# Performance work log

Measured on AMD Instinct MI355X. Metric: run time of the kernel, lower is better.

The kernel has to match this reference:

```python
import jax, jax.numpy as jnp
import numpy as np

NODE_FEATURES = 256
HIDDEN = 32
N_NODES = 100000
N_EDGES = 3200000


def _glorot(key, shape):
    fan_in, fan_out = shape[-2], shape[-1]
    lim = (6.0 / (fan_in + fan_out)) ** 0.5
    return jax.random.uniform(key, shape, jnp.float32, -lim, lim)


def setup_inputs() -> dict:
    key = jax.random.key(0)
    ks = jax.random.split(key, 12)
    in_cat = NODE_FEATURES + HIDDEN  # DConv input is cat([X, H])
    x = jax.random.normal(ks[0], (N_NODES, NODE_FEATURES), jnp.float32)
    edge_index = jax.random.randint(ks[1], (2, N_EDGES), 0, N_NODES, jnp.int64)
    return {
        "x": x,
        "edge_index": edge_index,
        # DConv weights have shape (2, K=1, in, out); squeeze K -> (2, in, out)
        "w_z": _glorot(ks[2], (2, in_cat, HIDDEN)),
        "b_z": jnp.zeros((HIDDEN,), jnp.float32),
        "w_r": _glorot(ks[3], (2, in_cat, HIDDEN)),
        "b_r": jnp.zeros((HIDDEN,), jnp.float32),
        "w_h": _glorot(ks[4], (2, in_cat, HIDDEN)),
        "b_h": jnp.zeros((HIDDEN,), jnp.float32),
        # fc head, stored as [in, out]
        "fc1_w": _glorot(ks[5], (HIDDEN, HIDDEN)),
        "fc1_b": jnp.zeros((HIDDEN,), jnp.float32),
        "fc2_w": _glorot(ks[6], (HIDDEN, 1)),
        "fc2_b": jnp.zeros((1,), jnp.float32),
    }


def _dconv_k1(inp, w, b):
    # K=1 DConv: only the k=0 Chebyshev term for both diffusion directions,
    # i.e. no propagation over edges. H = X @ W_out + X @ W_in + bias.
    return inp @ (w[0] + w[1]) + b


def reference(x, edge_index, w_z, b_z, w_r, b_r, w_h, b_h, fc1_w, fc1_b, fc2_w, fc2_b):
    n = x.shape[0]
    h0 = jnp.zeros((n, HIDDEN), x.dtype)  # DCRNN called with H=None -> zeros
    xh0 = jnp.concatenate([x, h0], axis=1)  # [N, F+H]
    z = jax.nn.sigmoid(_dconv_k1(xh0, w_z, b_z))  # update gate
    r = jax.nn.sigmoid(_dconv_k1(xh0, w_r, b_r))  # reset gate
    xrh = jnp.concatenate([x, r * h0], axis=1)
    h_tilde = jnp.tanh(_dconv_k1(xrh, w_h, b_h))
    h = z * h0 + (1.0 - z) * h_tilde  # [N, 32]
    # fc head: Linear-ReLU-Dropout(eval=identity)-Linear-Sigmoid
    hidden = jax.nn.relu(h @ fc1_w + fc1_b)
    out = jax.nn.sigmoid(hidden @ fc2_w + fc2_b)  # [N, 1]
    return out
```

## Files before the change

kernel.cpp:

```cpp
#include <hip/hip_runtime.h>
#include <hip/hip_bf16.h>


#define NF    256
#define TILE  32
#define WPB   4
#define MB    (TILE * WPB)
#define NTHR  256
#define HSTR  36

typedef __attribute__((ext_vector_type(8)))  short  short8;
typedef __attribute__((ext_vector_type(16))) float  floatx16;

__device__ __forceinline__ unsigned f2bf(float f) {
    __hip_bfloat16 h = __float2bfloat16(f);
    return (unsigned)*(unsigned short*)&h;
}
__device__ __forceinline__ float fast_sigmoid(float v) {
    return 1.0f / (1.0f + __expf(-v));
}
__device__ __forceinline__ float fast_tanh(float v) {
    return 1.0f - 2.0f / (1.0f + __expf(2.0f * v));
}

__global__ void prep_W(const float* __restrict__ wz,
                       const float* __restrict__ wh,
                       unsigned short* __restrict__ Wf)
{
    int idx = blockIdx.x * blockDim.x + threadIdx.x;
    if (idx >= NF * 64) return;
    int j    = idx & 7;
    int lane = (idx >> 3) & 63;
    int nt   = (idx >> 9) & 1;
    int kt   = idx >> 10;
    int k = kt * 16 + (lane >> 5) * 8 + j;
    int o = nt * 32 + (lane & 31);
    const int PLANE = 288 * 32;
    float v;
    if (o < 32) v = wz[k * 32 + o]        + wz[PLANE + k * 32 + o];
    else        v = wh[k * 32 + (o - 32)] + wh[PLANE + k * 32 + (o - 32)];
    Wf[idx] = (unsigned short)f2bf(v);
}

__global__ void __launch_bounds__(NTHR, 3)
rgcn_main(const float* __restrict__ x,
          const unsigned short* __restrict__ Wf,
          const float* __restrict__ bz,
          const float* __restrict__ bh,
          const float* __restrict__ fc1w,
          const float* __restrict__ fc1b,
          const float* __restrict__ fc2w,
          const float* __restrict__ fc2b,
          float* __restrict__ out,
          int n_nodes)
{
    __shared__ float Hs[WPB * TILE * HSTR];

    const int tid   = threadIdx.x;
    const int lane  = tid & 63;
    const int wave  = tid >> 6;
    const int node0 = blockIdx.x * MB + wave * TILE;

    const int m    = lane & 31;
    const int koff = (lane >> 5) * 8;
    int gn_a = node0 + m;
    if (gn_a >= n_nodes) gn_a = n_nodes - 1;
    const float* xr = x + (size_t)gn_a * NF + koff;

    floatx16 acc0 = {};
    floatx16 acc1 = {};

#pragma unroll
    for (int kt = 0; kt < 16; ++kt) {
        float4 v0 = *(const float4*)(xr + kt * 16);
        float4 v1 = *(const float4*)(xr + kt * 16 + 4);
        const uint4* bp = (const uint4*)Wf + (size_t)(kt * 2) * 64 + lane;
        uint4 b0u = bp[0];
        uint4 b1u = bp[64];
        union { short8 s; unsigned u[4]; } a, b0, b1;
        a.u[0] = f2bf(v0.x) | (f2bf(v0.y) << 16);
        a.u[1] = f2bf(v0.z) | (f2bf(v0.w) << 16);
        a.u[2] = f2bf(v1.x) | (f2bf(v1.y) << 16);
        a.u[3] = f2bf(v1.z) | (f2bf(v1.w) << 16);
        b0.u[0] = b0u.x; b0.u[1] = b0u.y; b0.u[2] = b0u.z; b0.u[3] = b0u.w;
        b1.u[0] = b1u.x; b1.u[1] = b1u.y; b1.u[2] = b1u.z; b1.u[3] = b1u.w;
        acc0 = __builtin_amdgcn_mfma_f32_32x32x16_bf16(a.s, b0.s, acc0, 0, 0, 0);
        acc1 = __builtin_amdgcn_mfma_f32_32x32x16_bf16(a.s, b1.s, acc1, 0, 0, 0);
    }

    const int nc = lane & 31;
    const float bzn = bz[nc];
    const float bhn = bh[nc];
    float* Hw = Hs + wave * TILE * HSTR;
#pragma unroll
    for (int r = 0; r < 16; ++r) {
        int row = (r & 3) + 8 * (r >> 2) + 4 * (lane >> 5);
        float z = fast_sigmoid(acc0[r] + bzn);
        float t = fast_tanh   (acc1[r] + bhn);
        Hw[row * HSTR + nc] = (1.0f - z) * t;
    }
    __syncthreads();

    const int nl   = lane & 31;
    const int half = lane >> 5;
    const float* hp = Hw + nl * HSTR;
    float h[32];
#pragma unroll
    for (int q = 0; q < 8; ++q) {
        float4 v = *(const float4*)(hp + q * 4);
        h[q * 4 + 0] = v.x; h[q * 4 + 1] = v.y;
        h[q * 4 + 2] = v.z; h[q * 4 + 3] = v.w;
    }
    float part = 0.0f;
    for (int jj = 0; jj < 16; ++jj) {
        int j = (half << 4) + jj;
        float s = fc1b[j];
#pragma unroll
        for (int o = 0; o < 32; ++o)
            s = fmaf(h[o], fc1w[o * 32 + j], s);
        part = fmaf(fmaxf(s, 0.0f), fc2w[j], part);
    }
    part += __shfl_xor(part, 32);
    if (half == 0) {
        int gn = node0 + nl;
        if (gn < n_nodes)
            out[gn] = fast_sigmoid(part + fc2b[0]);
    }
}

extern "C" void kernel_launch(void* const* d_in, const int* in_sizes, int n_in,
                              void* d_out, int out_size, void* d_ws, size_t ws_size,
                              hipStream_t stream) {
    const float* x    = (const float*)d_in[0];
    const float* wz   = (const float*)d_in[2];
    const float* bz   = (const float*)d_in[3];
    const float* wh   = (const float*)d_in[6];
    const float* bh   = (const float*)d_in[7];
    const float* fc1w = (const float*)d_in[8];
    const float* fc1b = (const float*)d_in[9];
    const float* fc2w = (const float*)d_in[10];
    const float* fc2b = (const float*)d_in[11];
    float* out = (float*)d_out;
    unsigned short* Wf = (unsigned short*)d_ws;

    const int n = in_sizes[0] / NF;

    prep_W<<<(NF * 64 + 255) / 256, 256, 0, stream>>>(wz, wh, Wf);
    rgcn_main<<<(n + MB - 1) / MB, NTHR, 0, stream>>>(
        x, Wf, bz, bh, fc1w, fc1b, fc2w, fc2b, out, n);
}
```

Baseline: 209.5 us.

## Stage x tiles into LDS via direct global-to-LDS loads in K chunks

Replaces the per-lane strided float4 loads of x rows with global_load_lds instructions that copy 256-byte row chunks directly into shared memory, then reads MFMA A-operands from LDS. K is split into 4 chunks, each followed by block barriers, with a padded group stride to limit bank conflicts. Launch bounds occupancy hint is raised from 3 to 4. The aim is better coalesced HBM access for this bandwidth-bound GEMV-like kernel, at the cost of extra barriers and no overlap between loading and compute within a block.

```diff
diff --git a/kernel.cpp b/kernel.cpp
--- a/kernel.cpp
+++ b/kernel.cpp
@@ -2,15 +2,18 @@
 #include <hip/hip_bf16.h>
 
 
-#define NF    256
-#define TILE  32
-#define WPB   4
-#define MB    (TILE * WPB)
-#define NTHR  256
-#define HSTR  36
+#define NF     256
+#define TILE   32
+#define WPB    4
+#define MB     (TILE * WPB)
+#define NTHR   256
+#define GRP    1040
+#define HSTR   36
 
 typedef __attribute__((ext_vector_type(8)))  short  short8;
 typedef __attribute__((ext_vector_type(16))) float  floatx16;
+typedef __attribute__((address_space(1))) const unsigned int gu32;
+typedef __attribute__((address_space(3))) unsigned int       lu32;
 
 __device__ __forceinline__ unsigned f2bf(float f) {
     __hip_bfloat16 h = __float2bfloat16(f);
@@ -42,7 +45,7 @@
     Wf[idx] = (unsigned short)f2bf(v);
 }
 
-__global__ void __launch_bounds__(NTHR, 3)
+__global__ void __launch_bounds__(NTHR, 4)
 rgcn_main(const float* __restrict__ x,
           const unsigned short* __restrict__ Wf,
           const float* __restrict__ bz,
@@ -54,44 +57,66 @@
           float* __restrict__ out,
           int n_nodes)
 {
-    __shared__ float Hs[WPB * TILE * HSTR];
+    __shared__ __align__(16) char S[32 * GRP];
 
     const int tid   = threadIdx.x;
     const int lane  = tid & 63;
     const int wave  = tid >> 6;
-    const int node0 = blockIdx.x * MB + wave * TILE;
+    const int node0 = blockIdx.x * MB;
+    const int wb    = wave * TILE;
 
-    const int m    = lane & 31;
+    const int rsel = lane >> 4;
+    const int cb   = (lane & 15) * 16;
+
+    const int m    = wb + (lane & 31);
     const int koff = (lane >> 5) * 8;
-    int gn_a = node0 + m;
-    if (gn_a >= n_nodes) gn_a = n_nodes - 1;
-    const float* xr = x + (size_t)gn_a * NF + koff;
+    const char* arow = S + (m >> 2) * GRP + (m & 3) * 256;
 
     floatx16 acc0 = {};
     floatx16 acc1 = {};
 
 #pragma unroll
-    for (int kt = 0; kt < 16; ++kt) {
-        float4 v0 = *(const float4*)(xr + kt * 16);
-        float4 v1 = *(const float4*)(xr + kt * 16 + 4);
-        const uint4* bp = (const uint4*)Wf + (size_t)(kt * 2) * 64 + lane;
-        uint4 b0u = bp[0];
-        uint4 b1u = bp[64];
-        union { short8 s; unsigned u[4]; } a, b0, b1;
-        a.u[0] = f2bf(v0.x) | (f2bf(v0.y) << 16);
-        a.u[1] = f2bf(v0.z) | (f2bf(v0.w) << 16);
-        a.u[2] = f2bf(v1.x) | (f2bf(v1.y) << 16);
-        a.u[3] = f2bf(v1.z) | (f2bf(v1.w) << 16);
-        b0.u[0] = b0u.x; b0.u[1] = b0u.y; b0.u[2] = b0u.z; b0.u[3] = b0u.w;
-        b1.u[0] = b1u.x; b1.u[1] = b1u.y; b1.u[2] = b1u.z; b1.u[3] = b1u.w;
-        acc0 = __builtin_amdgcn_mfma_f32_32x32x16_bf16(a.s, b0.s, acc0, 0, 0, 0);
-        acc1 = __builtin_amdgcn_mfma_f32_32x32x16_bf16(a.s, b1.s, acc1, 0, 0, 0);
+    for (int c = 0; c < 4; ++c) {
+        if (c) __syncthreads();
+#pragma unroll
+        for (int i = 0; i < 8; ++i) {
+            int inst = wave * 8 + i;
+            int row  = node0 + inst * 4 + rsel;
+            if (row >= n_nodes) row = n_nodes - 1;
+            const char* g = (const char*)x + (size_t)row * (NF * 4)
+                          + c * 256 + cb;
+            char* lp = S + inst * GRP;
+            __builtin_amdgcn_global_load_lds((gu32*)g, (lu32*)lp, 16, 0, 0);
+        }
+        __syncthreads();
+
+#pragma unroll
+        for (int kt = 0; kt < 4; ++kt) {
+            int ktg = c * 4 + kt;
+            const float4* ap = (const float4*)(arow + (kt * 16 + koff) * 4);
+            float4 v0 = ap[0];
+            float4 v1 = ap[1];
+            const uint4* bp = (const uint4*)Wf + (size_t)(ktg * 2) * 64 + lane;
+            uint4 b0u = bp[0];
+            uint4 b1u = bp[64];
+            union { short8 s; unsigned u[4]; } a, b0, b1;
+            a.u[0] = f2bf(v0.x) | (f2bf(v0.y) << 16);
+            a.u[1] = f2bf(v0.z) | (f2bf(v0.w) << 16);
+            a.u[2] = f2bf(v1.x) | (f2bf(v1.y) << 16);
+            a.u[3] = f2bf(v1.z) | (f2bf(v1.w) << 16);
+            b0.u[0] = b0u.x; b0.u[1] = b0u.y; b0.u[2] = b0u.z; b0.u[3] = b0u.w;
+            b1.u[0] = b1u.x; b1.u[1] = b1u.y; b1.u[2] = b1u.z; b1.u[3] = b1u.w;
+            acc0 = __builtin_amdgcn_mfma_f32_32x32x16_bf16(a.s, b0.s, acc0, 0, 0, 0);
+            acc1 = __builtin_amdgcn_mfma_f32_32x32x16_bf16(a.s, b1.s, acc1, 0, 0, 0);
+        }
     }
 
+    __syncthreads();
+    float* Hs = (float*)S;
+    float* Hw = Hs + wave * TILE * HSTR;
     const int nc = lane & 31;
     const float bzn = bz[nc];
     const float bhn = bh[nc];
-    float* Hw = Hs + wave * TILE * HSTR;
 #pragma unroll
     for (int r = 0; r < 16; ++r) {
         int row = (r & 3) + 8 * (r >> 2) + 4 * (lane >> 5);
@@ -122,7 +147,7 @@
     }
     part += __shfl_xor(part, 32);
     if (half == 0) {
-        int gn = node0 + nl;
+        int gn = node0 + wb + nl;
         if (gn < n_nodes)
             out[gn] = fast_sigmoid(part + fc2b[0]);
     }
```

After: 205.3 us. 1.02x faster.

## Stage weights in LDS and double-buffer x loads in register chunks

Applied to the files above, without the earlier changes.

Each block first copies the packed bf16 weight fragments (32 KB) into shared memory, using a padded group stride to spread banks, so the MFMA loop reads B operands from LDS instead of global memory. The x row loads are split into four 64-element chunks and double-buffered in registers, with sched_barriers that force the next chunk's loads to issue before the current chunk's MFMAs. The block-wide __syncthreads after the H tile write becomes a per-wave lgkmcnt wait, since each wave only reads its own tile. In exchange the kernel uses about 33 KB more LDS per block and more registers, which can reduce occupancy under launch_bounds(256,3), and every block pays a preamble copy plus a barrier.

```diff
diff --git a/kernel.cpp b/kernel.cpp
--- a/kernel.cpp
+++ b/kernel.cpp
@@ -7,6 +7,7 @@
 #define WPB   4
 #define MB    (TILE * WPB)
 #define NTHR  256
+#define BGRP  1040
 #define HSTR  36
 
 typedef __attribute__((ext_vector_type(8)))  short  short8;
@@ -54,44 +55,75 @@
           float* __restrict__ out,
           int n_nodes)
 {
+    __shared__ __align__(16) char SB[32 * BGRP];
     __shared__ float Hs[WPB * TILE * HSTR];
 
     const int tid   = threadIdx.x;
     const int lane  = tid & 63;
     const int wave  = tid >> 6;
-    const int node0 = blockIdx.x * MB + wave * TILE;
+    const int node0 = blockIdx.x * MB;
 
-    const int m    = lane & 31;
-    const int koff = (lane >> 5) * 8;
-    int gn_a = node0 + m;
+    {
+        const uint4* src = (const uint4*)Wf;
+#pragma unroll
+        for (int i = 0; i < 8; ++i) {
+            int q = i * NTHR + tid;
+            uint4 v = src[q];
+            *(uint4*)(SB + (q >> 6) * BGRP + (q & 63) * 16) = v;
+        }
+    }
+    __syncthreads();
+
+    const int m  = lane & 31;
+    int gn_a = node0 + wave * TILE + m;
     if (gn_a >= n_nodes) gn_a = n_nodes - 1;
-    const float* xr = x + (size_t)gn_a * NF + koff;
+    const float* xr = x + (size_t)gn_a * NF + (lane >> 5) * 8;
 
     floatx16 acc0 = {};
     floatx16 acc1 = {};
 
+    float4 bufA[8], bufB[8];
+    const char* bl = SB + lane * 16;
+
 #pragma unroll
-    for (int kt = 0; kt < 16; ++kt) {
-        float4 v0 = *(const float4*)(xr + kt * 16);
-        float4 v1 = *(const float4*)(xr + kt * 16 + 4);
-        const uint4* bp = (const uint4*)Wf + (size_t)(kt * 2) * 64 + lane;
-        uint4 b0u = bp[0];
-        uint4 b1u = bp[64];
-        union { short8 s; unsigned u[4]; } a, b0, b1;
-        a.u[0] = f2bf(v0.x) | (f2bf(v0.y) << 16);
-        a.u[1] = f2bf(v0.z) | (f2bf(v0.w) << 16);
-        a.u[2] = f2bf(v1.x) | (f2bf(v1.y) << 16);
-        a.u[3] = f2bf(v1.z) | (f2bf(v1.w) << 16);
-        b0.u[0] = b0u.x; b0.u[1] = b0u.y; b0.u[2] = b0u.z; b0.u[3] = b0u.w;
-        b1.u[0] = b1u.x; b1.u[1] = b1u.y; b1.u[2] = b1u.z; b1.u[3] = b1u.w;
-        acc0 = __builtin_amdgcn_mfma_f32_32x32x16_bf16(a.s, b0.s, acc0, 0, 0, 0);
-        acc1 = __builtin_amdgcn_mfma_f32_32x32x16_bf16(a.s, b1.s, acc1, 0, 0, 0);
+    for (int t = 0; t < 8; ++t)
+        bufA[t] = *(const float4*)(xr + (t >> 1) * 16 + (t & 1) * 4);
+    __builtin_amdgcn_sched_barrier(0);
+
+#pragma unroll
+    for (int c = 0; c < 4; ++c) {
+        if (c < 3) {
+            float4* nb = ((c & 1) == 0) ? bufB : bufA;
+            const float* xc = xr + (c + 1) * 64;
+#pragma unroll
+            for (int t = 0; t < 8; ++t)
+                nb[t] = *(const float4*)(xc + (t >> 1) * 16 + (t & 1) * 4);
+            __builtin_amdgcn_sched_barrier(0);
+        }
+        const float4* cb = ((c & 1) == 0) ? bufA : bufB;
+#pragma unroll
+        for (int kt = 0; kt < 4; ++kt) {
+            float4 v0 = cb[kt * 2];
+            float4 v1 = cb[kt * 2 + 1];
+            int g = (c * 4 + kt) * 2;
+            uint4 b0u = *(const uint4*)(bl + (size_t)g * BGRP);
+            uint4 b1u = *(const uint4*)(bl + (size_t)(g + 1) * BGRP);
+            union { short8 s; unsigned u[4]; } a, b0, b1;
+            a.u[0] = f2bf(v0.x) | (f2bf(v0.y) << 16);
+            a.u[1] = f2bf(v0.z) | (f2bf(v0.w) << 16);
+            a.u[2] = f2bf(v1.x) | (f2bf(v1.y) << 16);
+            a.u[3] = f2bf(v1.z) | (f2bf(v1.w) << 16);
+            b0.u[0] = b0u.x; b0.u[1] = b0u.y; b0.u[2] = b0u.z; b0.u[3] = b0u.w;
+            b1.u[0] = b1u.x; b1.u[1] = b1u.y; b1.u[2] = b1u.z; b1.u[3] = b1u.w;
+            acc0 = __builtin_amdgcn_mfma_f32_32x32x16_bf16(a.s, b0.s, acc0, 0, 0, 0);
+            acc1 = __builtin_amdgcn_mfma_f32_32x32x16_bf16(a.s, b1.s, acc1, 0, 0, 0);
+        }
     }
 
+    float* Hw = Hs + wave * TILE * HSTR;
     const int nc = lane & 31;
     const float bzn = bz[nc];
     const float bhn = bh[nc];
-    float* Hw = Hs + wave * TILE * HSTR;
 #pragma unroll
     for (int r = 0; r < 16; ++r) {
         int row = (r & 3) + 8 * (r >> 2) + 4 * (lane >> 5);
@@ -99,7 +131,7 @@
         float t = fast_tanh   (acc1[r] + bhn);
         Hw[row * HSTR + nc] = (1.0f - z) * t;
     }
-    __syncthreads();
+    asm volatile("s_waitcnt lgkmcnt(0)" ::: "memory");
 
     const int nl   = lane & 31;
     const int half = lane >> 5;
@@ -122,7 +154,7 @@
     }
     part += __shfl_xor(part, 32);
     if (half == 0) {
-        int gn = node0 + nl;
+        int gn = node0 + wave * TILE + nl;
         if (gn < n_nodes)
             out[gn] = fast_sigmoid(part + fc2b[0]);
     }
```

New measurement: 203.4 us. -2.9%, faster.

## Split K across waves with LDS reduction and nontemporal x loads

Applied to the files above, without the earlier changes.

Each block now handles 64 nodes, and the four waves are split into two node tiles times two K-halves. Each wave runs half the MFMA K loop, and the partial accumulators are reduced through shared memory before the gate epilogue and FC head. The intent is more waves in flight per node and higher memory-level parallelism on the bandwidth-bound x read, helped by nontemporal loads and a raised occupancy hint. The cost is extra LDS traffic, two more barriers, and half the waves sitting idle during the epilogue.

```diff
diff --git a/kernel.cpp b/kernel.cpp
--- a/kernel.cpp
+++ b/kernel.cpp
@@ -4,13 +4,14 @@
 
 #define NF    256
 #define TILE  32
-#define WPB   4
-#define MB    (TILE * WPB)
+#define NPB   64
 #define NTHR  256
-#define HSTR  36
+#define CSTR  68
+#define HKT   8
 
 typedef __attribute__((ext_vector_type(8)))  short  short8;
 typedef __attribute__((ext_vector_type(16))) float  floatx16;
+typedef __attribute__((ext_vector_type(4)))  float  f32x4;
 
 __device__ __forceinline__ unsigned f2bf(float f) {
     __hip_bfloat16 h = __float2bfloat16(f);
@@ -42,7 +43,7 @@
     Wf[idx] = (unsigned short)f2bf(v);
 }
 
-__global__ void __launch_bounds__(NTHR, 3)
+__global__ void __launch_bounds__(NTHR, 5)
 rgcn_main(const float* __restrict__ x,
           const unsigned short* __restrict__ Wf,
           const float* __restrict__ bz,
@@ -54,29 +55,30 @@
           float* __restrict__ out,
           int n_nodes)
 {
-    __shared__ float Hs[WPB * TILE * HSTR];
+    __shared__ __align__(16) float Xc[NPB * CSTR];
 
     const int tid   = threadIdx.x;
     const int lane  = tid & 63;
     const int wave  = tid >> 6;
-    const int node0 = blockIdx.x * MB + wave * TILE;
+    const int tile  = wave & 1;
+    const int khalf = wave >> 1;
+    const int node0 = blockIdx.x * NPB;
 
-    const int m    = lane & 31;
-    const int koff = (lane >> 5) * 8;
-    int gn_a = node0 + m;
-    if (gn_a >= n_nodes) gn_a = n_nodes - 1;
-    const float* xr = x + (size_t)gn_a * NF + koff;
+    const int nc = lane & 31;
+    int gn = node0 + tile * TILE + nc;
+    if (gn >= n_nodes) gn = n_nodes - 1;
+    const float* xr = x + (size_t)gn * NF + khalf * 128 + (lane >> 5) * 8;
 
     floatx16 acc0 = {};
     floatx16 acc1 = {};
 
 #pragma unroll
-    for (int kt = 0; kt < 16; ++kt) {
-        float4 v0 = *(const float4*)(xr + kt * 16);
-        float4 v1 = *(const float4*)(xr + kt * 16 + 4);
-        const uint4* bp = (const uint4*)Wf + (size_t)(kt * 2) * 64 + lane;
-        uint4 b0u = bp[0];
-        uint4 b1u = bp[64];
+    for (int kt = 0; kt < HKT; ++kt) {
+        f32x4 v0 = __builtin_nontemporal_load((const f32x4*)(xr + kt * 16));
+        f32x4 v1 = __builtin_nontemporal_load((const f32x4*)(xr + kt * 16 + 4));
+        int g = khalf * HKT + kt;
+        uint4 b0u = ((const uint4*)Wf)[(size_t)(g * 2 + 0) * 64 + lane];
+        uint4 b1u = ((const uint4*)Wf)[(size_t)(g * 2 + 1) * 64 + lane];
         union { short8 s; unsigned u[4]; } a, b0, b1;
         a.u[0] = f2bf(v0.x) | (f2bf(v0.y) << 16);
         a.u[1] = f2bf(v0.z) | (f2bf(v0.w) << 16);
@@ -88,43 +90,67 @@
         acc1 = __builtin_amdgcn_mfma_f32_32x32x16_bf16(a.s, b1.s, acc1, 0, 0, 0);
     }
 
-    const int nc = lane & 31;
-    const float bzn = bz[nc];
-    const float bhn = bh[nc];
-    float* Hw = Hs + wave * TILE * HSTR;
+    if (khalf == 1) {
 #pragma unroll
-    for (int r = 0; r < 16; ++r) {
-        int row = (r & 3) + 8 * (r >> 2) + 4 * (lane >> 5);
-        float z = fast_sigmoid(acc0[r] + bzn);
-        float t = fast_tanh   (acc1[r] + bhn);
-        Hw[row * HSTR + nc] = (1.0f - z) * t;
+        for (int r = 0; r < 16; ++r) {
+            int row = (r & 3) + 8 * (r >> 2) + 4 * (lane >> 5);
+            int base = (tile * TILE + row) * CSTR;
+            Xc[base + nc]      = acc0[r];
+            Xc[base + 32 + nc] = acc1[r];
+        }
     }
     __syncthreads();
 
-    const int nl   = lane & 31;
-    const int half = lane >> 5;
-    const float* hp = Hw + nl * HSTR;
-    float h[32];
+    if (khalf == 0) {
+        const float bzn = bz[nc];
+        const float bhn = bh[nc];
 #pragma unroll
-    for (int q = 0; q < 8; ++q) {
-        float4 v = *(const float4*)(hp + q * 4);
-        h[q * 4 + 0] = v.x; h[q * 4 + 1] = v.y;
-        h[q * 4 + 2] = v.z; h[q * 4 + 3] = v.w;
+        for (int r = 0; r < 16; ++r) {
+            int row = (r & 3) + 8 * (r >> 2) + 4 * (lane >> 5);
+            int base = (tile * TILE + row) * CSTR;
+            float s0 = acc0[r] + Xc[base + nc];
+            float s1 = acc1[r] + Xc[base + 32 + nc];
+            float z = fast_sigmoid(s0 + bzn);
+            float t = fast_tanh   (s1 + bhn);
+            acc0[r] = (1.0f - z) * t;
+        }
     }
-    float part = 0.0f;
-    for (int jj = 0; jj < 16; ++jj) {
-        int j = (half << 4) + jj;
-        float s = fc1b[j];
+    __syncthreads();
+    if (khalf == 0) {
 #pragma unroll
-        for (int o = 0; o < 32; ++o)
-            s = fmaf(h[o], fc1w[o * 32 + j], s);
-        part = fmaf(fmaxf(s, 0.0f), fc2w[j], part);
+        for (int r = 0; r < 16; ++r) {
+            int row = (r & 3) + 8 * (r >> 2) + 4 * (lane >> 5);
+            Xc[(tile * TILE + row) * CSTR + nc] = acc0[r];
+        }
     }
-    part += __shfl_xor(part, 32);
-    if (half == 0) {
-        int gn = node0 + nl;
-        if (gn < n_nodes)
-            out[gn] = fast_sigmoid(part + fc2b[0]);
+    __syncthreads();
+
+    if (khalf == 0) {
+        const int nl   = nc;
+        const int half = lane >> 5;
+        const float* hp = Xc + (tile * TILE + nl) * CSTR;
+        float h[32];
+#pragma unroll
+        for (int q = 0; q < 8; ++q) {
+            float4 v = *(const float4*)(hp + q * 4);
+            h[q * 4 + 0] = v.x; h[q * 4 + 1] = v.y;
+            h[q * 4 + 2] = v.z; h[q * 4 + 3] = v.w;
+        }
+        float part = 0.0f;
+        for (int jj = 0; jj < 16; ++jj) {
+            int j = (half << 4) + jj;
+            float s = fc1b[j];
+#pragma unroll
+            for (int o = 0; o < 32; ++o)
+                s = fmaf(h[o], fc1w[o * 32 + j], s);
+            part = fmaf(fmaxf(s, 0.0f), fc2w[j], part);
+        }
+        part += __shfl_xor(part, 32);
+        if (half == 0) {
+            int g = node0 + tile * TILE + nl;
+            if (g < n_nodes)
+                out[g] = fast_sigmoid(part + fc2b[0]);
+        }
     }
 }
 
@@ -146,6 +172,6 @@
     const int n = in_sizes[0] / NF;
 
     prep_W<<<(NF * 64 + 255) / 256, 256, 0, stream>>>(wz, wh, Wf);
-    rgcn_main<<<(n + MB - 1) / MB, NTHR, 0, stream>>>(
+    rgcn_main<<<(n + NPB - 1) / NPB, NTHR, 0, stream>>>(
         x, Wf, bz, bh, fc1w, fc1b, fc2w, fc2b, out, n);
 }
```

New measurement: 208.4 us. About the same (-0.5%).
